# Kernel tuning notes

Measured on AMD Instinct MI355X. Metric: run time of the kernel, lower is better.

## Reference

```python
import jax, jax.numpy as jnp
import numpy as np

N = 50000      # nodes
E = 640000     # edges
F_IN = 128     # in_channels
H = 128        # hidden / layer size
G = 64         # graphs in batch
OUT = 5        # classes


def _lin_init(key, fan_in, fan_out):
    s = 1.0 / np.sqrt(fan_in)
    kw, kb = jax.random.split(key)
    w = jax.random.uniform(kw, (fan_in, fan_out), jnp.float32, -s, s)
    b = jax.random.uniform(kb, (fan_out,), jnp.float32, -s, s)
    return w, b


def setup_inputs() -> dict:
    key = jax.random.key(0)
    ks = jax.random.split(key, 8)
    x = jax.random.normal(ks[0], (N, F_IN), jnp.float32)
    edge_index = jax.random.randint(ks[1], (2, E), 0, N, dtype=jnp.int64)
    # sorted graph assignment, every graph nonempty (sorted_randint-style)
    batch = (jnp.arange(N, dtype=jnp.int64) * G) // N
    c0w1, c0b1 = _lin_init(ks[2], F_IN, H)
    c0w2, c0b2 = _lin_init(ks[3], H, H)
    c1w1, c1b1 = _lin_init(ks[4], H, H)
    c1w2, c1b2 = _lin_init(ks[5], H, H)
    lw, lb = _lin_init(ks[6], H, OUT)
    return {"x": x, "edge_index": edge_index, "batch": batch,
            "conv0_w1": c0w1, "conv0_b1": c0b1, "conv0_w2": c0w2, "conv0_b2": c0b2,
            "conv1_w1": c1w1, "conv1_b1": c1b1, "conv1_w2": c1w2, "conv1_b2": c1b2,
            "lin_w": lw, "lin_b": lb}


def reference(x, edge_index, batch,
              conv0_w1, conv0_b1, conv0_w2, conv0_b2,
              conv1_w1, conv1_b1, conv1_w2, conv1_b2,
              lin_w, lin_b):
    src, dst = edge_index[0], edge_index[1]

    def gin_conv(h, w1, b1, w2, b2):
        # scatter-add neighbor aggregation: out_i = sum_{(j->i) in E} h_j
        agg = jax.ops.segment_sum(h[src], dst, num_segments=N)
        z = agg + h  # GIN with eps = 0 (train_eps=False)
        # PyG MLP (2 layers, eval mode): Linear -> ReLU -> Linear
        z = jax.nn.relu(z @ w1 + b1) @ w2 + b2
        return jax.nn.relu(z)  # outer .relu() in forward

    h = gin_conv(x, conv0_w1, conv0_b1, conv0_w2, conv0_b2)
    h = gin_conv(h, conv1_w1, conv1_b1, conv1_w2, conv1_b2)
    # global max pool over each graph (all segments nonempty by construction)
    pooled = jax.ops.segment_max(h, batch, num_segments=G)
    # dropout p=0.3 is a no-op in eval mode
    return pooled @ lin_w + lin_b
```

## Files before the change

### kernel.cpp

```cpp
#include <hip/hip_runtime.h>
#include <hip/hip_bf16.h>

#define N_NODES 50000
#define N_EDGES 640000
#define HDIM 128
#define NGRAPH 64
#define NOUT 5
#define CAP 64
#define CL 32

typedef __attribute__((ext_vector_type(4))) short short4v;
typedef __attribute__((ext_vector_type(8))) short short8v;
typedef __attribute__((ext_vector_type(4))) float float4v;

__device__ inline float blo(unsigned u) { return __uint_as_float(u << 16); }
__device__ inline float bhi(unsigned u) { return __uint_as_float(u & 0xffff0000u); }
__device__ inline unsigned short f2b(float f) {
    __hip_bfloat16 h = __float2bfloat16(f);
    return *reinterpret_cast<unsigned short*>(&h);
}

__device__ inline int xcd_swz(int bid, int n) {
    int x = bid & 7, d = bid >> 3;
    int q = n >> 3, rem = n & 7;
    return (x < rem) ? x * (q + 1) + d : rem * (q + 1) + (x - rem) * q + d;
}


__global__ void k_zero(int* __restrict__ p, int n) {
    int i = blockIdx.x * 256 + threadIdx.x;
    if (i < n) p[i] = 0;
}

__global__ __launch_bounds__(256) void k_prep(const float* __restrict__ x,
                                              const float* __restrict__ w0a,
                                              const float* __restrict__ w0b,
                                              const float* __restrict__ w1a,
                                              const float* __restrict__ w1b,
                                              const int* __restrict__ srcv,
                                              const int* __restrict__ dstv,
                                              int* __restrict__ cur,
                                              int* __restrict__ adj,
                                              unsigned short* __restrict__ wf,
                                              unsigned short* __restrict__ xb) {
    int i = blockIdx.x * 256 + threadIdx.x;
    if (i < N_EDGES) {
        int d = dstv[i];
        int pos = atomicAdd(&cur[(size_t)d * CL], 1);
        adj[(size_t)d * CAP + pos] = srcv[i];
    }
    if (i < 4 * 2048) {
        int m = i >> 11, rem = i & 2047;
        int c = rem >> 8, ks = (rem >> 6) & 3, lane = rem & 63;
        int r = lane & 15, g = lane >> 4;
        int n = c * 16 + r, k0 = ks * 32 + 4 * g;
        const float* w = (m == 0) ? w0a : (m == 1) ? w0b : (m == 2) ? w1a : w1b;
        unsigned short v[8];
#pragma unroll
        for (int j = 0; j < 4; j++) {
            v[j]     = f2b(w[(k0 + j) * HDIM + n]);
            v[4 + j] = f2b(w[(k0 + 16 + j) * HDIM + n]);
        }
        uint4 o;
        o.x = v[0] | ((unsigned)v[1] << 16);
        o.y = v[2] | ((unsigned)v[3] << 16);
        o.z = v[4] | ((unsigned)v[5] << 16);
        o.w = v[6] | ((unsigned)v[7] << 16);
        ((uint4*)wf)[i] = o;
    }
    if (i < N_NODES * 16) {
        int row = i >> 4;
        int p0 = (i & 15) * 8;
        int ks = p0 >> 5, g2 = (p0 >> 3) & 3;
        const float* xr = x + (size_t)row * HDIM + ks * 32 + 4 * g2;
        float4 a = *(const float4*)xr;
        float4 b = *(const float4*)(xr + 16);
        uint4 o;
        o.x = f2b(a.x) | ((unsigned)f2b(a.y) << 16);
        o.y = f2b(a.z) | ((unsigned)f2b(a.w) << 16);
        o.z = f2b(b.x) | ((unsigned)f2b(b.y) << 16);
        o.w = f2b(b.z) | ((unsigned)f2b(b.w) << 16);
        *(uint4*)&xb[(size_t)row * HDIM + p0] = o;
    }
}

__global__ __launch_bounds__(256) void k_agg_b(const unsigned short* __restrict__ h,
                                               const int* __restrict__ cnt,
                                               const int* __restrict__ adj,
                                               unsigned short* __restrict__ out) {
    int node = xcd_swz(blockIdx.x, gridDim.x) * 16 + (threadIdx.x >> 4);
    if (node >= N_NODES) return;
    int c = (threadIdx.x & 15) * 8;
    const unsigned short* hc = h + c;
    uint4 sv = *(const uint4*)(hc + (size_t)node * HDIM);
    float acc[8];
    acc[0] = blo(sv.x); acc[1] = bhi(sv.x);
    acc[2] = blo(sv.y); acc[3] = bhi(sv.y);
    acc[4] = blo(sv.z); acc[5] = bhi(sv.z);
    acc[6] = blo(sv.w); acc[7] = bhi(sv.w);
#define ACC8(v) do { \
        acc[0] += blo(v.x); acc[1] += bhi(v.x); \
        acc[2] += blo(v.y); acc[3] += bhi(v.y); \
        acc[4] += blo(v.z); acc[5] += bhi(v.z); \
        acc[6] += blo(v.w); acc[7] += bhi(v.w); } while (0)
    int s = node * CAP;
    int e = s + cnt[(size_t)node * CL];
    int k = s;
    for (; k + 4 <= e; k += 4) {
        int j0 = adj[k], j1 = adj[k + 1], j2 = adj[k + 2], j3 = adj[k + 3];
        uint4 v0 = *(const uint4*)(hc + (size_t)j0 * HDIM);
        uint4 v1 = *(const uint4*)(hc + (size_t)j1 * HDIM);
        uint4 v2 = *(const uint4*)(hc + (size_t)j2 * HDIM);
        uint4 v3 = *(const uint4*)(hc + (size_t)j3 * HDIM);
        ACC8(v0); ACC8(v1); ACC8(v2); ACC8(v3);
    }
    for (; k < e; k++) {
        int j = adj[k];
        uint4 v = *(const uint4*)(hc + (size_t)j * HDIM);
        ACC8(v);
    }
#undef ACC8
    uint4 o;
    o.x = f2b(acc[0]) | ((unsigned)f2b(acc[1]) << 16);
    o.y = f2b(acc[2]) | ((unsigned)f2b(acc[3]) << 16);
    o.z = f2b(acc[4]) | ((unsigned)f2b(acc[5]) << 16);
    o.w = f2b(acc[6]) | ((unsigned)f2b(acc[7]) << 16);
    *(uint4*)&out[(size_t)node * HDIM + c] = o;
}

template <bool POOL>
__global__ __launch_bounds__(256, 3) void k_mlp(const unsigned short* __restrict__ A,
                                                const unsigned short* __restrict__ w1f,
                                                const unsigned short* __restrict__ w2f,
                                                const float* __restrict__ b1,
                                                const float* __restrict__ b2,
                                                unsigned short* __restrict__ C,
                                                unsigned* __restrict__ pooled) {
    int tid = threadIdx.x;
    int lane = tid & 63;
    int w = tid >> 6;
    int r = lane & 15;
    int g = lane >> 4;
    int Lb = xcd_swz(blockIdx.x, gridDim.x);
    int base = Lb * 64 + w * 16;
    int row = base + r;
    int rowc = (row < N_NODES) ? row : (N_NODES - 1);

    const short8v* W1 = (const short8v*)w1f;
    const short8v* W2 = (const short8v*)w2f;

    short8v fbv[4];
    {
        const unsigned short* arow = A + (size_t)rowc * HDIM;
#pragma unroll
        for (int ks = 0; ks < 4; ks++)
            fbv[ks] = *(const short8v*)(arow + ks * 32 + g * 8);
    }

    float4v acc1[8];
#pragma unroll
    for (int c = 0; c < 8; c++) acc1[c] = (float4v){0.f, 0.f, 0.f, 0.f};
#pragma unroll
    for (int ks = 0; ks < 4; ks++) {
        short8v wfr[8];
#pragma unroll
        for (int c = 0; c < 8; c++) wfr[c] = W1[(c * 4 + ks) * 64 + lane];
#pragma unroll
        for (int c = 0; c < 8; c++)
            acc1[c] = __builtin_amdgcn_mfma_f32_16x16x32_bf16(wfr[c], fbv[ks], acc1[c], 0, 0, 0);
    }

    short8v fb2[4];
#pragma unroll
    for (int ks = 0; ks < 4; ks++) {
        float4 bA = *(const float4*)&b1[(2 * ks) * 16 + 4 * g];
        float4 bB = *(const float4*)&b1[(2 * ks + 1) * 16 + 4 * g];
        short8v f;
        f[0] = (short)f2b(fmaxf(acc1[2 * ks][0] + bA.x, 0.f));
        f[1] = (short)f2b(fmaxf(acc1[2 * ks][1] + bA.y, 0.f));
        f[2] = (short)f2b(fmaxf(acc1[2 * ks][2] + bA.z, 0.f));
        f[3] = (short)f2b(fmaxf(acc1[2 * ks][3] + bA.w, 0.f));
        f[4] = (short)f2b(fmaxf(acc1[2 * ks + 1][0] + bB.x, 0.f));
        f[5] = (short)f2b(fmaxf(acc1[2 * ks + 1][1] + bB.y, 0.f));
        f[6] = (short)f2b(fmaxf(acc1[2 * ks + 1][2] + bB.z, 0.f));
        f[7] = (short)f2b(fmaxf(acc1[2 * ks + 1][3] + bB.w, 0.f));
        fb2[ks] = f;
    }

    float4v acc2[8];
#pragma unroll
    for (int c = 0; c < 8; c++) acc2[c] = (float4v){0.f, 0.f, 0.f, 0.f};
#pragma unroll
    for (int ks = 0; ks < 4; ks++) {
        short8v wfr[8];
#pragma unroll
        for (int c = 0; c < 8; c++) wfr[c] = W2[(c * 4 + ks) * 64 + lane];
#pragma unroll
        for (int c = 0; c < 8; c++)
            acc2[c] = __builtin_amdgcn_mfma_f32_16x16x32_bf16(wfr[c], fb2[ks], acc2[c], 0, 0, 0);
    }

    if constexpr (!POOL) {
        bool ok = (row < N_NODES);
#pragma unroll
        for (int ks = 0; ks < 4; ks++) {
            float4 bA = *(const float4*)&b2[ks * 32 + 4 * g];
            float4 bB = *(const float4*)&b2[ks * 32 + 16 + 4 * g];
            uint4 st;
            st.x = f2b(fmaxf(acc2[2 * ks][0] + bA.x, 0.f)) |
                   ((unsigned)f2b(fmaxf(acc2[2 * ks][1] + bA.y, 0.f)) << 16);
            st.y = f2b(fmaxf(acc2[2 * ks][2] + bA.z, 0.f)) |
                   ((unsigned)f2b(fmaxf(acc2[2 * ks][3] + bA.w, 0.f)) << 16);
            st.z = f2b(fmaxf(acc2[2 * ks + 1][0] + bB.x, 0.f)) |
                   ((unsigned)f2b(fmaxf(acc2[2 * ks + 1][1] + bB.y, 0.f)) << 16);
            st.w = f2b(fmaxf(acc2[2 * ks + 1][2] + bB.z, 0.f)) |
                   ((unsigned)f2b(fmaxf(acc2[2 * ks + 1][3] + bB.w, 0.f)) << 16);
            if (ok) *(uint4*)&C[(size_t)row * HDIM + ks * 32 + g * 8] = st;
        }
    } else {
        unsigned gid0 = ((unsigned)base * 64u) / 50000u;
        unsigned gid1 = ((unsigned)(base + 15) * 64u) / 50000u;
        bool fast = (base + 15 < N_NODES) && (gid0 == gid1);
        if (fast) {
            float vm[8][4];
#pragma unroll
            for (int c = 0; c < 8; c++) {
                int ks = c >> 1, h2 = c & 1;
                float4 bv = *(const float4*)&b2[ks * 32 + h2 * 16 + 4 * g];
                float bb[4] = {bv.x, bv.y, bv.z, bv.w};
#pragma unroll
                for (int i = 0; i < 4; i++)
                    vm[c][i] = fmaxf(acc2[c][i] + bb[i], 0.f);
            }
#pragma unroll
            for (int mask = 1; mask <= 8; mask <<= 1)
#pragma unroll
                for (int c = 0; c < 8; c++)
#pragma unroll
                    for (int i = 0; i < 4; i++)
                        vm[c][i] = fmaxf(vm[c][i], __shfl_xor(vm[c][i], mask));
            if (r == 0) {
                unsigned* pool = pooled + gid0 * HDIM;
#pragma unroll
                for (int c = 0; c < 8; c++) {
                    int p = (c >> 1) * 32 + g * 8 + (c & 1) * 4;
#pragma unroll
                    for (int i = 0; i < 4; i++)
                        atomicMax(&pool[p + i], __float_as_uint(vm[c][i]));
                }
            }
        } else if (row < N_NODES) {
            unsigned gid = ((unsigned)row * 64u) / 50000u;
            unsigned* pool = pooled + gid * HDIM;
#pragma unroll
            for (int c = 0; c < 8; c++) {
                int ks = c >> 1, h2 = c & 1;
                float4 bv = *(const float4*)&b2[ks * 32 + h2 * 16 + 4 * g];
                float bb[4] = {bv.x, bv.y, bv.z, bv.w};
                int p = ks * 32 + g * 8 + h2 * 4;
#pragma unroll
                for (int i = 0; i < 4; i++)
                    atomicMax(&pool[p + i],
                              __float_as_uint(fmaxf(acc2[c][i] + bb[i], 0.f)));
            }
        }
    }
}

__global__ void k_final(const float* __restrict__ pooled, const float* __restrict__ lw,
                        const float* __restrict__ lb, float* __restrict__ out) {
    int t = threadIdx.x;
    if (t >= NGRAPH * NOUT) return;
    int g = t / NOUT, o = t % NOUT;
    float acc = lb[o];
    for (int p = 0; p < HDIM; p++) {
        int col = (p & 0x60) | ((p & 4) << 2) | ((p & 0x18) >> 1) | (p & 3);
        acc = fmaf(pooled[g * HDIM + p], lw[col * NOUT + o], acc);
    }
    out[t] = acc;
}

extern "C" void kernel_launch(void* const* d_in, const int* in_sizes, int n_in,
                              void* d_out, int out_size, void* d_ws, size_t ws_size,
                              hipStream_t stream) {
    const float* x    = (const float*)d_in[0];
    const int*   ei   = (const int*)d_in[1];
    const int*   srcv = ei;
    const int*   dstv = ei + N_EDGES;
    const float* c0w1 = (const float*)d_in[3];
    const float* c0b1 = (const float*)d_in[4];
    const float* c0w2 = (const float*)d_in[5];
    const float* c0b2 = (const float*)d_in[6];
    const float* c1w1 = (const float*)d_in[7];
    const float* c1b1 = (const float*)d_in[8];
    const float* c1w2 = (const float*)d_in[9];
    const float* c1b2 = (const float*)d_in[10];
    const float* lw   = (const float*)d_in[11];
    const float* lb   = (const float*)d_in[12];
    float* out = (float*)d_out;

    char* ws = (char*)d_ws;
    int* cur      = (int*)(ws);
    float* pooled = (float*)(cur + (size_t)N_NODES * CL);
    int* adj      = (int*)(ws + 8ull * 1024 * 1024);
    unsigned short* wf = (unsigned short*)(ws + 21ull * 1024 * 1024);
    unsigned short* xb = (unsigned short*)(ws + 22ull * 1024 * 1024);
    unsigned short* b0 = (unsigned short*)(ws + 35ull * 1024 * 1024);
    unsigned short* b1 = (unsigned short*)(ws + 48ull * 1024 * 1024);

    const int NZ  = N_NODES * CL + NGRAPH * HDIM;
    const int NBZ = (NZ + 255) / 256;
    const int NBL = (N_NODES + 63) / 64;
    const int NBA = (N_NODES + 15) / 16;
    const int NBC = (N_NODES * 16 + 255) / 256;

    k_zero<<<NBZ, 256, 0, stream>>>(cur, NZ);

    k_prep<<<NBC, 256, 0, stream>>>(x, c0w1, c0w2, c1w1, c1w2,
                                    srcv, dstv, cur, adj, wf, xb);

    k_agg_b<<<NBA, 256, 0, stream>>>(xb, cur, adj, b0);
    k_mlp<false><<<NBL, 256, 0, stream>>>(b0, wf, wf + 16384, c0b1, c0b2, b1, nullptr);

    k_agg_b<<<NBA, 256, 0, stream>>>(b1, cur, adj, b0);
    k_mlp<true><<<NBL, 256, 0, stream>>>(b0, wf + 32768, wf + 49152, c1b1, c1b2,
                                         nullptr, (unsigned*)pooled);

    k_final<<<1, 320, 0, stream>>>(pooled, lw, lb, out);
}
```

Before: 240.3 us.

## Split MLP output columns across waves with LDS exchange of hidden activations

The MLP kernel now processes 16 rows per block, with each of the four waves computing 32 output columns instead of one wave computing all 128 columns for its own 16 rows. The first-layer hidden activations are exchanged through a padded shared-memory tile and a block barrier before the second layer. This cuts per-wave accumulator and weight-fragment registers so occupancy can rise (launch bounds raised to 4). In exchange it adds a barrier and LDS traffic per block, and it drops row-bounds checks on the assumption that N is divisible by 16.

```diff
diff --git a/kernel.cpp b/kernel.cpp
--- a/kernel.cpp
+++ b/kernel.cpp
@@ -129,140 +129,128 @@
 }
 
 template <bool POOL>
-__global__ __launch_bounds__(256, 3) void k_mlp(const unsigned short* __restrict__ A,
+__global__ __launch_bounds__(256, 4) void k_mlp(const unsigned short* __restrict__ A,
                                                 const unsigned short* __restrict__ w1f,
                                                 const unsigned short* __restrict__ w2f,
                                                 const float* __restrict__ b1,
                                                 const float* __restrict__ b2,
                                                 unsigned short* __restrict__ C,
                                                 unsigned* __restrict__ pooled) {
+    __shared__ uint4 z1[16 * 17];
     int tid = threadIdx.x;
     int lane = tid & 63;
     int w = tid >> 6;
     int r = lane & 15;
     int g = lane >> 4;
-    int Lb = xcd_swz(blockIdx.x, gridDim.x);
-    int base = Lb * 64 + w * 16;
+    int base = xcd_swz(blockIdx.x, gridDim.x) * 16;
     int row = base + r;
-    int rowc = (row < N_NODES) ? row : (N_NODES - 1);
 
     const short8v* W1 = (const short8v*)w1f;
     const short8v* W2 = (const short8v*)w2f;
 
     short8v fbv[4];
     {
-        const unsigned short* arow = A + (size_t)rowc * HDIM;
+        const unsigned short* arow = A + (size_t)row * HDIM;
 #pragma unroll
         for (int ks = 0; ks < 4; ks++)
             fbv[ks] = *(const short8v*)(arow + ks * 32 + g * 8);
     }
 
-    float4v acc1[8];
-#pragma unroll
-    for (int c = 0; c < 8; c++) acc1[c] = (float4v){0.f, 0.f, 0.f, 0.f};
-#pragma unroll
-    for (int ks = 0; ks < 4; ks++) {
+    float4v acc1[2];
+    acc1[0] = (float4v){0.f, 0.f, 0.f, 0.f};
+    acc1[1] = (float4v){0.f, 0.f, 0.f, 0.f};
+    {
         short8v wfr[8];
 #pragma unroll
-        for (int c = 0; c < 8; c++) wfr[c] = W1[(c * 4 + ks) * 64 + lane];
-#pragma unroll
-        for (int c = 0; c < 8; c++)
-            acc1[c] = __builtin_amdgcn_mfma_f32_16x16x32_bf16(wfr[c], fbv[ks], acc1[c], 0, 0, 0);
-    }
+        for (int ks = 0; ks < 4; ks++) {
+            wfr[2 * ks]     = W1[((2 * w) * 4 + ks) * 64 + lane];
+            wfr[2 * ks + 1] = W1[((2 * w + 1) * 4 + ks) * 64 + lane];
+        }
+#pragma unroll
+        for (int ks = 0; ks < 4; ks++) {
+            acc1[0] = __builtin_amdgcn_mfma_f32_16x16x32_bf16(wfr[2 * ks],     fbv[ks], acc1[0], 0, 0, 0);
+            acc1[1] = __builtin_amdgcn_mfma_f32_16x16x32_bf16(wfr[2 * ks + 1], fbv[ks], acc1[1], 0, 0, 0);
+        }
+    }
+
+    {
+        float4 bA = *(const float4*)&b1[(2 * w) * 16 + 4 * g];
+        float4 bB = *(const float4*)&b1[(2 * w + 1) * 16 + 4 * g];
+        uint4 z;
+        z.x = f2b(fmaxf(acc1[0][0] + bA.x, 0.f)) |
+              ((unsigned)f2b(fmaxf(acc1[0][1] + bA.y, 0.f)) << 16);
+        z.y = f2b(fmaxf(acc1[0][2] + bA.z, 0.f)) |
+              ((unsigned)f2b(fmaxf(acc1[0][3] + bA.w, 0.f)) << 16);
+        z.z = f2b(fmaxf(acc1[1][0] + bB.x, 0.f)) |
+              ((unsigned)f2b(fmaxf(acc1[1][1] + bB.y, 0.f)) << 16);
+        z.w = f2b(fmaxf(acc1[1][2] + bB.z, 0.f)) |
+              ((unsigned)f2b(fmaxf(acc1[1][3] + bB.w, 0.f)) << 16);
+        z1[r * 17 + w * 4 + g] = z;
+    }
+    __syncthreads();
 
     short8v fb2[4];
 #pragma unroll
-    for (int ks = 0; ks < 4; ks++) {
-        float4 bA = *(const float4*)&b1[(2 * ks) * 16 + 4 * g];
-        float4 bB = *(const float4*)&b1[(2 * ks + 1) * 16 + 4 * g];
-        short8v f;
-        f[0] = (short)f2b(fmaxf(acc1[2 * ks][0] + bA.x, 0.f));
-        f[1] = (short)f2b(fmaxf(acc1[2 * ks][1] + bA.y, 0.f));
-        f[2] = (short)f2b(fmaxf(acc1[2 * ks][2] + bA.z, 0.f));
-        f[3] = (short)f2b(fmaxf(acc1[2 * ks][3] + bA.w, 0.f));
-        f[4] = (short)f2b(fmaxf(acc1[2 * ks + 1][0] + bB.x, 0.f));
-        f[5] = (short)f2b(fmaxf(acc1[2 * ks + 1][1] + bB.y, 0.f));
-        f[6] = (short)f2b(fmaxf(acc1[2 * ks + 1][2] + bB.z, 0.f));
-        f[7] = (short)f2b(fmaxf(acc1[2 * ks + 1][3] + bB.w, 0.f));
-        fb2[ks] = f;
-    }
-
-    float4v acc2[8];
-#pragma unroll
-    for (int c = 0; c < 8; c++) acc2[c] = (float4v){0.f, 0.f, 0.f, 0.f};
-#pragma unroll
-    for (int ks = 0; ks < 4; ks++) {
+    for (int ks = 0; ks < 4; ks++)
+        fb2[ks] = *(const short8v*)&z1[r * 17 + ks * 4 + g];
+
+    float4v acc2[2];
+    acc2[0] = (float4v){0.f, 0.f, 0.f, 0.f};
+    acc2[1] = (float4v){0.f, 0.f, 0.f, 0.f};
+    {
         short8v wfr[8];
 #pragma unroll
-        for (int c = 0; c < 8; c++) wfr[c] = W2[(c * 4 + ks) * 64 + lane];
-#pragma unroll
-        for (int c = 0; c < 8; c++)
-            acc2[c] = __builtin_amdgcn_mfma_f32_16x16x32_bf16(wfr[c], fb2[ks], acc2[c], 0, 0, 0);
-    }
+        for (int ks = 0; ks < 4; ks++) {
+            wfr[2 * ks]     = W2[((2 * w) * 4 + ks) * 64 + lane];
+            wfr[2 * ks + 1] = W2[((2 * w + 1) * 4 + ks) * 64 + lane];
+        }
+#pragma unroll
+        for (int ks = 0; ks < 4; ks++) {
+            acc2[0] = __builtin_amdgcn_mfma_f32_16x16x32_bf16(wfr[2 * ks],     fb2[ks], acc2[0], 0, 0, 0);
+            acc2[1] = __builtin_amdgcn_mfma_f32_16x16x32_bf16(wfr[2 * ks + 1], fb2[ks], acc2[1], 0, 0, 0);
+        }
+    }
+
+    float4 bA = *(const float4*)&b2[(2 * w) * 16 + 4 * g];
+    float4 bB = *(const float4*)&b2[(2 * w + 1) * 16 + 4 * g];
+    float v8[8];
+    v8[0] = fmaxf(acc2[0][0] + bA.x, 0.f);
+    v8[1] = fmaxf(acc2[0][1] + bA.y, 0.f);
+    v8[2] = fmaxf(acc2[0][2] + bA.z, 0.f);
+    v8[3] = fmaxf(acc2[0][3] + bA.w, 0.f);
+    v8[4] = fmaxf(acc2[1][0] + bB.x, 0.f);
+    v8[5] = fmaxf(acc2[1][1] + bB.y, 0.f);
+    v8[6] = fmaxf(acc2[1][2] + bB.z, 0.f);
+    v8[7] = fmaxf(acc2[1][3] + bB.w, 0.f);
 
     if constexpr (!POOL) {
-        bool ok = (row < N_NODES);
-#pragma unroll
-        for (int ks = 0; ks < 4; ks++) {
-            float4 bA = *(const float4*)&b2[ks * 32 + 4 * g];
-            float4 bB = *(const float4*)&b2[ks * 32 + 16 + 4 * g];
-            uint4 st;
-            st.x = f2b(fmaxf(acc2[2 * ks][0] + bA.x, 0.f)) |
-                   ((unsigned)f2b(fmaxf(acc2[2 * ks][1] + bA.y, 0.f)) << 16);
-            st.y = f2b(fmaxf(acc2[2 * ks][2] + bA.z, 0.f)) |
-                   ((unsigned)f2b(fmaxf(acc2[2 * ks][3] + bA.w, 0.f)) << 16);
-            st.z = f2b(fmaxf(acc2[2 * ks + 1][0] + bB.x, 0.f)) |
-                   ((unsigned)f2b(fmaxf(acc2[2 * ks + 1][1] + bB.y, 0.f)) << 16);
-            st.w = f2b(fmaxf(acc2[2 * ks + 1][2] + bB.z, 0.f)) |
-                   ((unsigned)f2b(fmaxf(acc2[2 * ks + 1][3] + bB.w, 0.f)) << 16);
-            if (ok) *(uint4*)&C[(size_t)row * HDIM + ks * 32 + g * 8] = st;
-        }
+        uint4 st;
+        st.x = f2b(v8[0]) | ((unsigned)f2b(v8[1]) << 16);
+        st.y = f2b(v8[2]) | ((unsigned)f2b(v8[3]) << 16);
+        st.z = f2b(v8[4]) | ((unsigned)f2b(v8[5]) << 16);
+        st.w = f2b(v8[6]) | ((unsigned)f2b(v8[7]) << 16);
+        *(uint4*)&C[(size_t)row * HDIM + w * 32 + g * 8] = st;
     } else {
         unsigned gid0 = ((unsigned)base * 64u) / 50000u;
         unsigned gid1 = ((unsigned)(base + 15) * 64u) / 50000u;
-        bool fast = (base + 15 < N_NODES) && (gid0 == gid1);
-        if (fast) {
-            float vm[8][4];
-#pragma unroll
-            for (int c = 0; c < 8; c++) {
-                int ks = c >> 1, h2 = c & 1;
-                float4 bv = *(const float4*)&b2[ks * 32 + h2 * 16 + 4 * g];
-                float bb[4] = {bv.x, bv.y, bv.z, bv.w};
-#pragma unroll
-                for (int i = 0; i < 4; i++)
-                    vm[c][i] = fmaxf(acc2[c][i] + bb[i], 0.f);
+        if (gid0 == gid1) {
+#pragma unroll
+            for (int mask = 1; mask <= 8; mask <<= 1)
+#pragma unroll
+                for (int i = 0; i < 8; i++)
+                    v8[i] = fmaxf(v8[i], __shfl_xor(v8[i], mask));
+            if (r == 0) {
+                unsigned* pool = pooled + gid0 * HDIM + w * 32 + g * 8;
+#pragma unroll
+                for (int i = 0; i < 8; i++)
+                    atomicMax(&pool[i], __float_as_uint(v8[i]));
             }
-#pragma unroll
-            for (int mask = 1; mask <= 8; mask <<= 1)
-#pragma unroll
-                for (int c = 0; c < 8; c++)
-#pragma unroll
-                    for (int i = 0; i < 4; i++)
-                        vm[c][i] = fmaxf(vm[c][i], __shfl_xor(vm[c][i], mask));
-            if (r == 0) {
-                unsigned* pool = pooled + gid0 * HDIM;
-#pragma unroll
-                for (int c = 0; c < 8; c++) {
-                    int p = (c >> 1) * 32 + g * 8 + (c & 1) * 4;
-#pragma unroll
-                    for (int i = 0; i < 4; i++)
-                        atomicMax(&pool[p + i], __float_as_uint(vm[c][i]));
-                }
-            }
-        } else if (row < N_NODES) {
+        } else {
             unsigned gid = ((unsigned)row * 64u) / 50000u;
-            unsigned* pool = pooled + gid * HDIM;
-#pragma unroll
-            for (int c = 0; c < 8; c++) {
-                int ks = c >> 1, h2 = c & 1;
-                float4 bv = *(const float4*)&b2[ks * 32 + h2 * 16 + 4 * g];
-                float bb[4] = {bv.x, bv.y, bv.z, bv.w};
-                int p = ks * 32 + g * 8 + h2 * 4;
-#pragma unroll
-                for (int i = 0; i < 4; i++)
-                    atomicMax(&pool[p + i],
-                              __float_as_uint(fmaxf(acc2[c][i] + bb[i], 0.f)));
-            }
+            unsigned* pool = pooled + gid * HDIM + w * 32 + g * 8;
+#pragma unroll
+            for (int i = 0; i < 8; i++)
+                atomicMax(&pool[i], __float_as_uint(v8[i]));
         }
     }
 }
@@ -310,7 +298,7 @@
 
     const int NZ  = N_NODES * CL + NGRAPH * HDIM;
     const int NBZ = (NZ + 255) / 256;
-    const int NBL = (N_NODES + 63) / 64;
+    const int NBL = N_NODES / 16;
     const int NBA = (N_NODES + 15) / 16;
     const int NBC = (N_NODES * 16 + 255) / 256;
 
```

Measured after the change: 251.6 us. 1.05x slower.
